# Performance work log

Hardware: AMD Instinct MI355X
Metric: run time of the kernel (lower is better)

## Reference

```python
import jax, jax.numpy as jnp
import numpy as np


def conv2d(x, w, b, stride, pad):
    y = jax.lax.conv_general_dilated(
        x, w, (stride, stride), [(pad, pad), (pad, pad)],
        dimension_numbers=('NCHW', 'OIHW', 'NCHW'))
    return y + b[None, :, None, None]


def setup_inputs() -> dict:
    key = jax.random.key(0)
    ks = jax.random.split(key, 12)
    B = 8
    s = 0.02
    return {
        'x1': jax.random.normal(ks[0], (B, 256, 128, 128), jnp.float32),
        'x2': jax.random.normal(ks[1], (B, 512, 64, 64), jnp.float32),
        'x3': jax.random.normal(ks[2], (B, 1024, 32, 32), jnp.float32),
        'x4': jax.random.normal(ks[3], (B, 2048, 16, 16), jnp.float32),
        'cov1_w': jax.random.normal(ks[4], (512, 256, 3, 3), jnp.float32) * s,
        'cov1_b': jnp.zeros((512,), jnp.float32),
        'cov2_w': jax.random.normal(ks[5], (512, 512, 3, 3), jnp.float32) * s,
        'cov2_b': jnp.zeros((512,), jnp.float32),
        'cov3_w': jax.random.normal(ks[6], (512, 1024, 3, 3), jnp.float32) * s,
        'cov3_b': jnp.zeros((512,), jnp.float32),
        'cov4_w': jax.random.normal(ks[7], (512, 2048, 1, 1), jnp.float32) * s,
        'cov4_b': jnp.zeros((512,), jnp.float32),
        'gce_fc1_w': jax.random.normal(ks[8], (8, 64, 256), jnp.float32) * s,
        'gce_fc1_b': jnp.zeros((8, 64), jnp.float32),
        'gce_fc2_w': jax.random.normal(ks[9], (8, 256, 64), jnp.float32) * s,
        'gce_fc2_b': jnp.zeros((8, 256), jnp.float32),
        'gce_sa_w': jax.random.normal(ks[10], (8, 256), jnp.float32) * s,
        'gce_sa_b': jnp.zeros((8,), jnp.float32),
    }


def reference(x1, x2, x3, x4,
              cov1_w, cov1_b, cov2_w, cov2_b, cov3_w, cov3_b, cov4_w, cov4_b,
              gce_fc1_w, gce_fc1_b, gce_fc2_w, gce_fc2_b, gce_sa_w, gce_sa_b):
    # NOTE (faithful to original): DSCA.forward overwrites its attention output
    # with `rearrange(x, 'b (h w) c -> b c h w')`, i.e. it returns its first
    # argument (cov4(x4)) unchanged. Hence cov1/cov2/cov3 and the whole
    # dynamic-top-k attention path are dead code with exactly-zero gradients;
    # omitting them yields identical outputs and identical (zero) grads.
    x4 = conv2d(x4, cov4_w, cov4_b, 1, 0)          # [B,512,16,16]
    x = jnp.concatenate([x4, x4, x4, x4], axis=1)  # [B,2048,16,16]
    x0 = x
    B, C, H, W = x.shape
    G = 8
    xg = x.reshape(B, G, C // G, H, W)             # [B,G,256,H,W]
    # ChannelAttention per group (reduction_ratio=4: 256->64->256)
    avg = xg.mean(axis=(3, 4))                                           # [B,G,256]
    h = jax.nn.relu(jnp.einsum('bgc,goc->bgo', avg, gce_fc1_w) + gce_fc1_b)
    ca = jax.nn.sigmoid(jnp.einsum('bgo,gco->bgc', h, gce_fc2_w) + gce_fc2_b)
    y = xg * ca[:, :, :, None, None]
    # SpatialAttention per group (1x1 conv to 1 channel)
    sa = jax.nn.sigmoid(jnp.einsum('bgchw,gc->bghw', y, gce_sa_w)
                        + gce_sa_b[None, :, None, None])
    y = y * sa[:, :, None, :, :]
    # GroupCBAMEnhancer gating: sigmoid, then hard-1 above per-group mean
    y = jax.nn.sigmoid(y)
    mean = y.mean(axis=(2, 3, 4), keepdims=True)   # mean over (c,h,w) per group
    mask = jnp.where(y > mean, jnp.float32(1.0), y).reshape(B, C, H, W)
    return x * mask + x0
```

## Files before the change

kernel.cpp:

```cpp
#include <hip/hip_runtime.h>
#include <math.h>

typedef __attribute__((ext_vector_type(8))) short bf16x8;
typedef __attribute__((ext_vector_type(8))) unsigned short u16x8;
typedef __attribute__((ext_vector_type(4))) float f32x4;

__device__ __forceinline__ unsigned short f2bf(float f) {
    unsigned int u = __builtin_bit_cast(unsigned int, f);
    unsigned int r = (u + 0x7FFFu + ((u >> 16) & 1)) >> 16;
    return (unsigned short)r;
}

__device__ __forceinline__ float sigmoidf_(float v) {
    return 1.f / (1.f + expf(-v));
}

struct StageRegs { float4 w0, w1, x0, x1; };

__global__ __launch_bounds__(256, 4) void gemm_fused(
    const float* __restrict__ x4, const float* __restrict__ w,
    const float* __restrict__ bias, float* __restrict__ y4,
    float* __restrict__ chanpart)
{
    __shared__ short As[2][2048];
    __shared__ short Bs[2][2048];

    const int tid = threadIdx.x;
    const int wave = tid >> 6, lane = tid & 63;
    const int wm = wave >> 1, wn = wave & 1;
    const int lr = lane & 15, lh = lane >> 4;

    const int flat = blockIdx.x;
    const int b = flat & 7;
    const int j = flat >> 3;
    const int mt = j & 15;
    const int nq = j >> 4;

    const int ar = tid >> 3, ac = tid & 7;
    const int xu = tid >> 3, xp4 = tid & 7;

    const float* wbase = w + (size_t)(mt * 32 + ar) * 2048 + ac * 8;
    const float* xbase = x4 + ((size_t)b * 2048 + 2 * xu) * 256 + nq * 32 + xp4 * 4;

#define LOADT(R, t) {                                                         \
        (R).w0 = *(const float4*)(wbase + (t) * 64);                          \
        (R).w1 = *(const float4*)(wbase + (t) * 64 + 4);                      \
        (R).x0 = *(const float4*)(xbase + (size_t)(t) * 64 * 256);            \
        (R).x1 = *(const float4*)(xbase + (size_t)(t) * 64 * 256 + 256); }
#define WRITET(buf, R) {                                                      \
        u16x8 o;                                                              \
        o[0] = f2bf((R).w0.x); o[1] = f2bf((R).w0.y);                         \
        o[2] = f2bf((R).w0.z); o[3] = f2bf((R).w0.w);                         \
        o[4] = f2bf((R).w1.x); o[5] = f2bf((R).w1.y);                         \
        o[6] = f2bf((R).w1.z); o[7] = f2bf((R).w1.w);                         \
        *(u16x8*)(&As[buf][ar * 64 + ((ac ^ (ar & 7)) * 8)]) = o;             \
        unsigned int pk0 = f2bf((R).x0.x) | ((unsigned int)f2bf((R).x1.x) << 16); \
        unsigned int pk1 = f2bf((R).x0.y) | ((unsigned int)f2bf((R).x1.y) << 16); \
        unsigned int pk2 = f2bf((R).x0.z) | ((unsigned int)f2bf((R).x1.z) << 16); \
        unsigned int pk3 = f2bf((R).x0.w) | ((unsigned int)f2bf((R).x1.w) << 16); \
        unsigned int* bs32 = (unsigned int*)&Bs[buf][0];                      \
        { int p = xp4 * 4 + 0;                                                \
          bs32[p * 32 + ((xu >> 2) ^ (p & 7)) * 4 + (xu & 3)] = pk0; }        \
        { int p = xp4 * 4 + 1;                                                \
          bs32[p * 32 + ((xu >> 2) ^ (p & 7)) * 4 + (xu & 3)] = pk1; }        \
        { int p = xp4 * 4 + 2;                                                \
          bs32[p * 32 + ((xu >> 2) ^ (p & 7)) * 4 + (xu & 3)] = pk2; }        \
        { int p = xp4 * 4 + 3;                                                \
          bs32[p * 32 + ((xu >> 2) ^ (p & 7)) * 4 + (xu & 3)] = pk3; } }
#define MFMA_TILE(cur) {                                                      \
        _Pragma("unroll")                                                     \
        for (int kc = 0; kc < 2; ++kc) {                                      \
            const int ch = kc * 4 + lh;                                       \
            int rA = wm * 16 + lr, rB = wn * 16 + lr;                         \
            bf16x8 a0 = *(const bf16x8*)(&As[cur][rA * 64 + ((ch ^ (rA & 7)) * 8)]); \
            bf16x8 b0 = *(const bf16x8*)(&Bs[cur][rB * 64 + ((ch ^ (rB & 7)) * 8)]); \
            acc = __builtin_amdgcn_mfma_f32_16x16x32_bf16(a0, b0, acc, 0, 0, 0); \
        } }

    StageRegs Ra, Rb;
    LOADT(Ra, 0);
    WRITET(0, Ra);
    LOADT(Rb, 1);
    LOADT(Ra, 2);
    __syncthreads();

    f32x4 acc = {};
    for (int t = 0; t < 32; t += 2) {
        WRITET(1, Rb);
        if (t < 29) LOADT(Rb, t + 3);
        MFMA_TILE(0);
        __syncthreads();
        if (t < 30) {
            WRITET(0, Ra);
            if (t < 28) LOADT(Ra, t + 4);
        }
        MFMA_TILE(1);
        __syncthreads();
    }
#undef LOADT
#undef WRITET
#undef MFMA_TILE

    float* yb = y4 + ((size_t)b * 512 + mt * 32) * 256 + nq * 32;
#pragma unroll
    for (int rr = 0; rr < 4; ++rr) {
        const int m = wm * 16 + lh * 4 + rr;
        const float bv = bias[mt * 32 + m];
        yb[m * 256 + wn * 16 + lr] = acc[rr] + bv;
        float s = acc[rr];
        s += __shfl_xor(s, 1);
        s += __shfl_xor(s, 2);
        s += __shfl_xor(s, 4);
        s += __shfl_xor(s, 8);
        if (lr == 0)
            chanpart[(size_t)(b * 512 + mt * 32 + m) * 16 + nq * 2 + wn] = s + 16.f * bv;
    }
}

__global__ __launch_bounds__(256) void sa_kernel(
    const float* __restrict__ y4, const float* __restrict__ chanpart,
    const float* __restrict__ fc1w, const float* __restrict__ fc1b,
    const float* __restrict__ fc2w, const float* __restrict__ fc2b,
    const float* __restrict__ saw, const float* __restrict__ sab,
    float* __restrict__ ca, float* __restrict__ sa, float* __restrict__ gsums)
{
    const int blk = blockIdx.x;
    const int bg = blk >> 3, pc = blk & 7;
    const int b = bg >> 3, g = bg & 7;
    const int tid = threadIdx.x;
    const float* xg = y4 + ((size_t)b * 512 + (g & 1) * 256) * 256 + pc * 32;

    __shared__ float xl[256][32];
    __shared__ float avgs[256], red[256], hs[64], cas[256], caws[256], sas[32];

#pragma unroll
    for (int i = 0; i < 8; ++i) {
        int f = i * 256 + tid;
        int c = f >> 3, p4 = f & 7;
        float4 v = *(const float4*)(xg + c * 256 + p4 * 4);
        *(float4*)(&xl[c][p4 * 4]) = v;
    }
    {
        const float* cpp = chanpart + (size_t)(b * 512 + (g & 1) * 256 + tid) * 16;
        float cp = 0.f;
#pragma unroll
        for (int i = 0; i < 16; ++i) cp += cpp[i];
        avgs[tid] = cp * (1.f / 256.f);
    }
    __syncthreads();
    {
        int o = tid & 63, seg = tid >> 6;
        const float* wr = fc1w + (g * 64 + o) * 256 + seg * 64;
        const float* av = avgs + seg * 64;
        float s = 0.f;
#pragma unroll
        for (int i = 0; i < 64; ++i) s = fmaf(av[i], wr[i], s);
        red[tid] = s;
    }
    __syncthreads();
    if (tid < 64) {
        float s = fc1b[g * 64 + tid] + red[tid] + red[64 + tid] + red[128 + tid] + red[192 + tid];
        hs[tid] = fmaxf(s, 0.f);
    }
    __syncthreads();
    {
        const float* wr = fc2w + (g * 256 + tid) * 64;
        float s = fc2b[g * 256 + tid];
#pragma unroll
        for (int i = 0; i < 64; ++i) s = fmaf(hs[i], wr[i], s);
        float v = sigmoidf_(s);
        cas[tid] = v;
        caws[tid] = v * saw[g * 256 + tid];
        if (pc == 0) ca[bg * 256 + tid] = v;
    }
    __syncthreads();
    const int p_l = tid & 31, seg8 = tid >> 5;
    {
        float s = 0.f;
#pragma unroll
        for (int i = 0; i < 32; ++i) {
            int c = seg8 * 32 + i;
            s = fmaf(xl[c][p_l], caws[c], s);
        }
        red[tid] = s;
    }
    __syncthreads();
    if (tid < 32) {
        float s = sab[g];
#pragma unroll
        for (int k = 0; k < 8; ++k) s += red[k * 32 + tid];
        float v = sigmoidf_(s);
        sas[tid] = v;
        sa[bg * 256 + pc * 32 + tid] = v;
    }
    __syncthreads();
    {
        float sv = sas[p_l];
        float s = 0.f;
#pragma unroll
        for (int i = 0; i < 32; ++i) {
            int c = seg8 * 32 + i;
            s += sigmoidf_(xl[c][p_l] * cas[c] * sv);
        }
        red[tid] = s;
    }
    __syncthreads();
    for (int off = 128; off > 0; off >>= 1) {
        if (tid < off) red[tid] += red[tid + off];
        __syncthreads();
    }
    if (tid == 0) gsums[blk] = red[0];
}

__global__ __launch_bounds__(256) void final_kernel(
    const float* __restrict__ y4, const float* __restrict__ ca,
    const float* __restrict__ sa, const float* __restrict__ gsums,
    float* __restrict__ out)
{
    int f = blockIdx.x * 256 + threadIdx.x;
    int p4 = f & 63, ch = (f >> 6) & 2047, b = f >> 17;
    int g = ch >> 8, c = ch & 255, bg = b * 8 + g;
    const float4 x = *(const float4*)(y4 + ((size_t)b * 512 + (g & 1) * 256 + c) * 256 + p4 * 4);
    float cav = ca[bg * 256 + c];
    const float4 sv = *(const float4*)(sa + bg * 256 + p4 * 4);
    float msum = 0.f;
#pragma unroll
    for (int i = 0; i < 8; ++i) msum += gsums[bg * 8 + i];
    float mean = msum * (1.f / 65536.f);
    float4 o;
#define DOLANE(X) { float yv = sigmoidf_(x.X * cav * sv.X); float mk = (yv > mean) ? 1.f : yv; o.X = x.X * (1.f + mk); }
    DOLANE(x) DOLANE(y) DOLANE(z) DOLANE(w)
#undef DOLANE
    *(float4*)(out + (size_t)f * 4) = o;
}

extern "C" void kernel_launch(void* const* d_in, const int* in_sizes, int n_in,
                              void* d_out, int out_size, void* d_ws, size_t ws_size,
                              hipStream_t stream) {
    const float* x4   = (const float*)d_in[3];
    const float* w4   = (const float*)d_in[10];
    const float* b4   = (const float*)d_in[11];
    const float* fc1w = (const float*)d_in[12];
    const float* fc1b = (const float*)d_in[13];
    const float* fc2w = (const float*)d_in[14];
    const float* fc2b = (const float*)d_in[15];
    const float* saw  = (const float*)d_in[16];
    const float* sab  = (const float*)d_in[17];
    float* out = (float*)d_out;

    float* ws = (float*)d_ws;
    float* y4       = ws;
    float* ca       = ws + 1048576;
    float* saBuf    = ws + 1064960;
    float* gsums    = ws + 1081344;
    float* chanpart = ws + 1081856;

    gemm_fused<<<dim3(1024), dim3(256), 0, stream>>>(x4, w4, b4, y4, chanpart);
    sa_kernel<<<dim3(512), dim3(256), 0, stream>>>(y4, chanpart, fc1w, fc1b, fc2w, fc2b,
                                                   saw, sab, ca, saBuf, gsums);
    final_kernel<<<dim3(4096), dim3(256), 0, stream>>>(y4, ca, saBuf, gsums, out);
}
```

Before: 49.59 us.

## Enlarge GEMM block tile to 64x64 with 512 threads and two MFMAs per wave

The cov4 GEMM block tile grows from 32x32 to 64x64 outputs, with 512 threads per block and a quarter as many blocks. Each wave now issues two MFMAs that reuse one A fragment, and the per-channel partial sums shrink from 16 to 8 slots per channel, so sa_kernel reads fewer of them. This cuts redundant global loads and bf16 conversions of the weights and activations. In exchange the grid falls to 256 blocks, which may leave compute units underused, and shared memory per block doubles.

```diff
diff --git a/kernel.cpp b/kernel.cpp
--- a/kernel.cpp
+++ b/kernel.cpp
@@ -17,13 +17,13 @@
 
 struct StageRegs { float4 w0, w1, x0, x1; };
 
-__global__ __launch_bounds__(256, 4) void gemm_fused(
+__global__ __launch_bounds__(512) void gemm_fused(
     const float* __restrict__ x4, const float* __restrict__ w,
     const float* __restrict__ bias, float* __restrict__ y4,
     float* __restrict__ chanpart)
 {
-    __shared__ short As[2][2048];
-    __shared__ short Bs[2][2048];
+    __shared__ short As[2][4096];
+    __shared__ short Bs[2][4096];
 
     const int tid = threadIdx.x;
     const int wave = tid >> 6, lane = tid & 63;
@@ -33,14 +33,14 @@
     const int flat = blockIdx.x;
     const int b = flat & 7;
     const int j = flat >> 3;
-    const int mt = j & 15;
-    const int nq = j >> 4;
+    const int mt = j & 7;
+    const int nq = j >> 3;
 
     const int ar = tid >> 3, ac = tid & 7;
-    const int xu = tid >> 3, xp4 = tid & 7;
-
-    const float* wbase = w + (size_t)(mt * 32 + ar) * 2048 + ac * 8;
-    const float* xbase = x4 + ((size_t)b * 2048 + 2 * xu) * 256 + nq * 32 + xp4 * 4;
+    const int ku = tid >> 4, xp4 = tid & 15;
+
+    const float* wbase = w + (size_t)(mt * 64 + ar) * 2048 + ac * 8;
+    const float* xbase = x4 + ((size_t)b * 2048 + 2 * ku) * 256 + nq * 64 + xp4 * 4;
 
 #define LOADT(R, t) {                                                         \
         (R).w0 = *(const float4*)(wbase + (t) * 64);                          \
@@ -60,21 +60,24 @@
         unsigned int pk3 = f2bf((R).x0.w) | ((unsigned int)f2bf((R).x1.w) << 16); \
         unsigned int* bs32 = (unsigned int*)&Bs[buf][0];                      \
         { int p = xp4 * 4 + 0;                                                \
-          bs32[p * 32 + ((xu >> 2) ^ (p & 7)) * 4 + (xu & 3)] = pk0; }        \
+          bs32[p * 32 + ((ku >> 2) ^ (p & 7)) * 4 + (ku & 3)] = pk0; }        \
         { int p = xp4 * 4 + 1;                                                \
-          bs32[p * 32 + ((xu >> 2) ^ (p & 7)) * 4 + (xu & 3)] = pk1; }        \
+          bs32[p * 32 + ((ku >> 2) ^ (p & 7)) * 4 + (ku & 3)] = pk1; }        \
         { int p = xp4 * 4 + 2;                                                \
-          bs32[p * 32 + ((xu >> 2) ^ (p & 7)) * 4 + (xu & 3)] = pk2; }        \
+          bs32[p * 32 + ((ku >> 2) ^ (p & 7)) * 4 + (ku & 3)] = pk2; }        \
         { int p = xp4 * 4 + 3;                                                \
-          bs32[p * 32 + ((xu >> 2) ^ (p & 7)) * 4 + (xu & 3)] = pk3; } }
+          bs32[p * 32 + ((ku >> 2) ^ (p & 7)) * 4 + (ku & 3)] = pk3; } }
 #define MFMA_TILE(cur) {                                                      \
         _Pragma("unroll")                                                     \
         for (int kc = 0; kc < 2; ++kc) {                                      \
             const int ch = kc * 4 + lh;                                       \
-            int rA = wm * 16 + lr, rB = wn * 16 + lr;                         \
-            bf16x8 a0 = *(const bf16x8*)(&As[cur][rA * 64 + ((ch ^ (rA & 7)) * 8)]); \
-            bf16x8 b0 = *(const bf16x8*)(&Bs[cur][rB * 64 + ((ch ^ (rB & 7)) * 8)]); \
-            acc = __builtin_amdgcn_mfma_f32_16x16x32_bf16(a0, b0, acc, 0, 0, 0); \
+            int rA  = wm * 16 + lr;                                           \
+            int rB0 = wn * 32 + lr, rB1 = rB0 + 16;                           \
+            bf16x8 a0 = *(const bf16x8*)(&As[cur][rA  * 64 + ((ch ^ (rA  & 7)) * 8)]); \
+            bf16x8 b0 = *(const bf16x8*)(&Bs[cur][rB0 * 64 + ((ch ^ (rB0 & 7)) * 8)]); \
+            bf16x8 b1 = *(const bf16x8*)(&Bs[cur][rB1 * 64 + ((ch ^ (rB1 & 7)) * 8)]); \
+            acc0 = __builtin_amdgcn_mfma_f32_16x16x32_bf16(a0, b0, acc0, 0, 0, 0); \
+            acc1 = __builtin_amdgcn_mfma_f32_16x16x32_bf16(a0, b1, acc1, 0, 0, 0); \
         } }
 
     StageRegs Ra, Rb;
@@ -84,7 +87,7 @@
     LOADT(Ra, 2);
     __syncthreads();
 
-    f32x4 acc = {};
+    f32x4 acc0 = {}, acc1 = {};
     for (int t = 0; t < 32; t += 2) {
         WRITET(1, Rb);
         if (t < 29) LOADT(Rb, t + 3);
@@ -101,19 +104,20 @@
 #undef WRITET
 #undef MFMA_TILE
 
-    float* yb = y4 + ((size_t)b * 512 + mt * 32) * 256 + nq * 32;
+    float* yb = y4 + ((size_t)b * 512 + mt * 64) * 256 + nq * 64;
 #pragma unroll
     for (int rr = 0; rr < 4; ++rr) {
         const int m = wm * 16 + lh * 4 + rr;
-        const float bv = bias[mt * 32 + m];
-        yb[m * 256 + wn * 16 + lr] = acc[rr] + bv;
-        float s = acc[rr];
+        const float bv = bias[mt * 64 + m];
+        yb[m * 256 + wn * 32 + lr]      = acc0[rr] + bv;
+        yb[m * 256 + wn * 32 + 16 + lr] = acc1[rr] + bv;
+        float s = acc0[rr] + acc1[rr];
         s += __shfl_xor(s, 1);
         s += __shfl_xor(s, 2);
         s += __shfl_xor(s, 4);
         s += __shfl_xor(s, 8);
         if (lr == 0)
-            chanpart[(size_t)(b * 512 + mt * 32 + m) * 16 + nq * 2 + wn] = s + 16.f * bv;
+            chanpart[(size_t)(b * 512 + mt * 64 + m) * 8 + nq * 2 + wn] = s + 32.f * bv;
     }
 }
 
@@ -141,10 +145,10 @@
         *(float4*)(&xl[c][p4 * 4]) = v;
     }
     {
-        const float* cpp = chanpart + (size_t)(b * 512 + (g & 1) * 256 + tid) * 16;
+        const float* cpp = chanpart + (size_t)(b * 512 + (g & 1) * 256 + tid) * 8;
         float cp = 0.f;
 #pragma unroll
-        for (int i = 0; i < 16; ++i) cp += cpp[i];
+        for (int i = 0; i < 8; ++i) cp += cpp[i];
         avgs[tid] = cp * (1.f / 256.f);
     }
     __syncthreads();
@@ -255,7 +259,7 @@
     float* gsums    = ws + 1081344;
     float* chanpart = ws + 1081856;
 
-    gemm_fused<<<dim3(1024), dim3(256), 0, stream>>>(x4, w4, b4, y4, chanpart);
+    gemm_fused<<<dim3(256), dim3(512), 0, stream>>>(x4, w4, b4, y4, chanpart);
     sa_kernel<<<dim3(512), dim3(256), 0, stream>>>(y4, chanpart, fc1w, fc1b, fc2w, fc2b,
                                                    saw, sab, ca, saBuf, gsums);
     final_kernel<<<dim3(4096), dim3(256), 0, stream>>>(y4, ca, saBuf, gsums, out);
```

New measurement: 45.63 us. 1.09x faster.
